# Optimization experiments

Hardware: AMD Instinct MI355X
Metric: run time of the kernel (lower is better)

The kernel has to match this reference:

```python
import jax, jax.numpy as jnp
import numpy as np


def setup_inputs() -> dict:
    key = jax.random.key(0)
    ks = jax.random.split(key, 4)
    C, Cb = 256, 32  # in_channels, bottleneck = C // 8
    B, H, W = 4, 64, 64
    x = jax.random.normal(ks[0], (B, C, H, W), dtype=jnp.float32)
    Wq = jax.random.normal(ks[1], (Cb, C), dtype=jnp.float32) * 0.05
    Wk = jax.random.normal(ks[2], (Cb, C), dtype=jnp.float32) * 0.05
    Wv = jax.random.normal(ks[3], (C, C), dtype=jnp.float32) * 0.05
    return {
        "x": x,
        "Wq": Wq, "bq": jnp.zeros((Cb,), jnp.float32),
        "Wk": Wk, "bk": jnp.zeros((Cb,), jnp.float32),
        "Wv": Wv, "bv": jnp.zeros((C,), jnp.float32),
    }


def reference(x, Wq, bq, Wk, bk, Wv, bv):
    B, C, H, W = x.shape
    N = H * W
    xf = x.reshape(B, C, N)  # [B, C, N]
    # 1x1 convs == channel matmuls
    q = jnp.einsum('oc,bcn->bon', Wq, xf) + bq[None, :, None]  # [B, Cb, N]
    k = jnp.einsum('oc,bcn->bon', Wk, xf) + bk[None, :, None]  # [B, Cb, N]
    v = jnp.einsum('oc,bcn->bon', Wv, xf) + bv[None, :, None]  # [B, C, N]
    # attention[b, n, m] = sum_d q[b, d, n] * k[b, d, m]
    attn = jnp.einsum('bdn,bdm->bnm', q, k)  # [B, N, N]
    attn = jax.nn.softmax(attn, axis=-1)
    # out[b, c, n] = sum_m v[b, c, m] * attn[b, m, n]
    out = jnp.einsum('bcm,bmn->bcn', v, attn).reshape(B, C, H, W)
    return out + x
```

## Files before the change

### kernel.cpp

```cpp
#include <hip/hip_runtime.h>
#include <hip/hip_bf16.h>

#define B_  4
#define C_  256
#define CB_ 32
#define N_  4096

typedef short bf16x8 __attribute__((ext_vector_type(8)));
typedef float f32x4  __attribute__((ext_vector_type(4)));
typedef float f32x16 __attribute__((ext_vector_type(16)));

static __device__ __forceinline__ bf16x8 ld_bf8(const __hip_bfloat16* p) {
    return *reinterpret_cast<const bf16x8*>(p);
}
static __device__ __forceinline__ unsigned pk2(float a, float b) {
    union { __hip_bfloat16 h[2]; unsigned u; } z;
    z.h[0] = __float2bfloat16(a); z.h[1] = __float2bfloat16(b);
    return z.u;
}


__global__ __launch_bounds__(256) void wconv(
    const float* __restrict__ Wq, const float* __restrict__ Wk,
    const float* __restrict__ Wv, __hip_bfloat16* __restrict__ Wc)
{
    int idx = (blockIdx.x * 256 + threadIdx.x) * 4;
    if (idx >= 320 * 256) return;
    int o = idx >> 8, c = idx & 255;
    const float* src = o < 32 ? Wq + o * 256 + c
                     : o < 64 ? Wk + (o - 32) * 256 + c
                              : Wv + (o - 64) * 256 + c;
    float4 f = *reinterpret_cast<const float4*>(src);
    union { __hip_bfloat16 h[4]; uint2 u; } pk;
    pk.h[0] = __float2bfloat16(f.x); pk.h[1] = __float2bfloat16(f.y);
    pk.h[2] = __float2bfloat16(f.z); pk.h[3] = __float2bfloat16(f.w);
    *reinterpret_cast<uint2*>(Wc + idx) = pk.u;
}

__global__ __launch_bounds__(256) void qkv_gemm(
    const float* __restrict__ x, const __hip_bfloat16* __restrict__ Wc,
    const float* __restrict__ bq, const float* __restrict__ bk,
    const float* __restrict__ bv,
    __hip_bfloat16* __restrict__ qt, __hip_bfloat16* __restrict__ kt,
    __hip_bfloat16* __restrict__ v)
{
    const int b = blockIdx.y, n0 = blockIdx.x * 32;
    const int tid = threadIdx.x, lane = tid & 63, w = tid >> 6;
    const int lg = lane >> 4, lr = lane & 15;
    __shared__ __attribute__((aligned(16))) __hip_bfloat16 T[2][32][40];
    const float* xb = x + (size_t)b * C_ * N_;

    f32x4 acc[5][2] = {};
    for (int s = 0; s < 8; ++s) {
        const int c0 = s * 32, buf = s & 1;
        {
            int cl = tid >> 3, n4 = (tid & 7) * 4;
            float4 f = *reinterpret_cast<const float4*>(
                &xb[(size_t)(c0 + cl) * N_ + n0 + n4]);
            T[buf][n4 + 0][cl] = __float2bfloat16(f.x);
            T[buf][n4 + 1][cl] = __float2bfloat16(f.y);
            T[buf][n4 + 2][cl] = __float2bfloat16(f.z);
            T[buf][n4 + 3][cl] = __float2bfloat16(f.w);
        }
        __syncthreads();
        bf16x8 bfr[2];
#pragma unroll
        for (int nf = 0; nf < 2; ++nf)
            bfr[nf] = *reinterpret_cast<const bf16x8*>(&T[buf][nf * 16 + lr][lg * 8]);
#pragma unroll
        for (int t = 0; t < 5; ++t) {
            const int of = w + 4 * t;
            bf16x8 af = ld_bf8(Wc + (size_t)(of * 16 + lr) * 256 + c0 + lg * 8);
#pragma unroll
            for (int nf = 0; nf < 2; ++nf)
                acc[t][nf] = __builtin_amdgcn_mfma_f32_16x16x32_bf16(af, bfr[nf], acc[t][nf], 0, 0, 0);
        }
        __syncthreads();
    }
#pragma unroll
    for (int t = 0; t < 5; ++t) {
        const int of = w + 4 * t, ob = of * 16 + lg * 4;
        float bias[4];
#pragma unroll
        for (int i = 0; i < 4; ++i) {
            int o = ob + i;
            bias[i] = o < 32 ? bq[o] : o < 64 ? bk[o - 32] : bv[o - 64];
        }
#pragma unroll
        for (int nf = 0; nf < 2; ++nf) {
            const int n = n0 + nf * 16 + lr;
            if (ob < 64) {
                union { __hip_bfloat16 h[4]; uint2 u; } pk;
#pragma unroll
                for (int i = 0; i < 4; ++i)
                    pk.h[i] = __float2bfloat16(acc[t][nf][i] + bias[i]);
                __hip_bfloat16* dst = ob < 32
                    ? qt + ((size_t)b * N_ + n) * CB_ + ob
                    : kt + ((size_t)b * N_ + n) * CB_ + (ob - 32);
                *reinterpret_cast<uint2*>(dst) = pk.u;
            } else {
                const size_t pbase = ((size_t)(b * (N_ / 32) + (n0 >> 5)) * C_);
#pragma unroll
                for (int i = 0; i < 4; ++i)
                    v[(pbase + (ob - 64 + i)) * 32 + nf * 16 + lr] =
                        __float2bfloat16(acc[t][nf][i] + bias[i]);
            }
        }
    }
}

__global__ __launch_bounds__(256) void row_stats_part(
    const __hip_bfloat16* __restrict__ qt, const __hip_bfloat16* __restrict__ kt,
    float* __restrict__ pM, float* __restrict__ pZ)
{
    const int m0 = blockIdx.x * 64, s = blockIdx.y, b = blockIdx.z;
    const int tid = threadIdx.x, lane = tid & 63, w = tid >> 6;
    const int lg = lane >> 4, lr = lane & 15;
    const __hip_bfloat16* qtb = qt + (size_t)b * N_ * CB_;
    const __hip_bfloat16* ktb = kt + (size_t)b * N_ * CB_;
    const int mrow = m0 + w * 16;
    bf16x8 qf = ld_bf8(qtb + (size_t)(mrow + lr) * CB_ + lg * 8);
    float rm[4] = {-1e30f, -1e30f, -1e30f, -1e30f};
    float rz[4] = {0.f, 0.f, 0.f, 0.f};
    const f32x4 zero = {0.f, 0.f, 0.f, 0.f};
    const int nbeg = s * (N_ / 4);
    for (int n = nbeg; n < nbeg + N_ / 4; n += 64) {
        f32x4 sf[4];
#pragma unroll
        for (int nf = 0; nf < 4; ++nf) {
            bf16x8 kf = ld_bf8(ktb + (size_t)(n + nf * 16 + lr) * CB_ + lg * 8);
            sf[nf] = __builtin_amdgcn_mfma_f32_16x16x32_bf16(qf, kf, zero, 0, 0, 0);
        }
#pragma unroll
        for (int i = 0; i < 4; ++i) {
            float tm = fmaxf(fmaxf(sf[0][i], sf[1][i]), fmaxf(sf[2][i], sf[3][i]));
            if (tm > rm[i]) { rz[i] *= __expf(rm[i] - tm); rm[i] = tm; }
            rz[i] += __expf(sf[0][i] - rm[i]) + __expf(sf[1][i] - rm[i]) +
                     __expf(sf[2][i] - rm[i]) + __expf(sf[3][i] - rm[i]);
        }
    }
#pragma unroll
    for (int off = 1; off < 16; off <<= 1) {
#pragma unroll
        for (int i = 0; i < 4; ++i) {
            float om = __shfl_xor(rm[i], off);
            float oz = __shfl_xor(rz[i], off);
            float nm = fmaxf(rm[i], om);
            rz[i] = rz[i] * __expf(rm[i] - nm) + oz * __expf(om - nm);
            rm[i] = nm;
        }
    }
    if (lr == 0) {
        const size_t base = ((size_t)s * B_ + b) * N_ + mrow + lg * 4;
#pragma unroll
        for (int i = 0; i < 4; ++i) { pM[base + i] = rm[i]; pZ[base + i] = rz[i]; }
    }
}

__global__ __launch_bounds__(256) void stats_combine(
    const float* __restrict__ pM, const float* __restrict__ pZ,
    float* __restrict__ rowE)
{
    const int i = blockIdx.x * 256 + threadIdx.x;
    const int BN = B_ * N_;
    float m0 = pM[i], m1 = pM[BN + i], m2 = pM[2 * BN + i], m3 = pM[3 * BN + i];
    float M = fmaxf(fmaxf(m0, m1), fmaxf(m2, m3));
    float Z = pZ[i]          * __expf(m0 - M) + pZ[BN + i]     * __expf(m1 - M)
            + pZ[2 * BN + i] * __expf(m2 - M) + pZ[3 * BN + i] * __expf(m3 - M);
    rowE[i] = M + logf(Z);
}

#define QS 4096
#define VS 32768

#define PV_BODY(qC0, qC1, vC, qN0, qN1, vN, qpN, vpN, DO_LOAD)                  \
  {                                                                             \
    f32x4 e0 = *reinterpret_cast<const f32x4*>(ep + mcur);                      \
    f32x4 e1 = *reinterpret_cast<const f32x4*>(ep + mcur + 8);                  \
    f32x4 e2 = *reinterpret_cast<const f32x4*>(ep + mcur + 16);                 \
    f32x4 e3 = *reinterpret_cast<const f32x4*>(ep + mcur + 24);                 \
    if (DO_LOAD) {                                                              \
      qN0 = ld_bf8(qpN); qN1 = ld_bf8(qpN + 16);                                \
      _Pragma("unroll")                                                         \
      for (int ct = 0; ct < 4; ++ct) {                                          \
        vN[ct][0] = ld_bf8(vpN[ct]); vN[ct][1] = ld_bf8(vpN[ct] + 16);          \
      }                                                                         \
      qpN += 2 * QS;                                                            \
      _Pragma("unroll")                                                         \
      for (int ct = 0; ct < 4; ++ct) vpN[ct] += 2 * VS;                         \
    }                                                                           \
    f32x16 sf = {};                                                             \
    sf = __builtin_amdgcn_mfma_f32_32x32x16_bf16(qC0, kB0, sf, 0, 0, 0);        \
    sf = __builtin_amdgcn_mfma_f32_32x32x16_bf16(qC1, kB1, sf, 0, 0, 0);        \
    unsigned W0 = pk2(__expf(sf[0]  - e0[0]), __expf(sf[1]  - e0[1]));          \
    unsigned W1 = pk2(__expf(sf[2]  - e0[2]), __expf(sf[3]  - e0[3]));          \
    unsigned W2 = pk2(__expf(sf[4]  - e1[0]), __expf(sf[5]  - e1[1]));          \
    unsigned W3 = pk2(__expf(sf[6]  - e1[2]), __expf(sf[7]  - e1[3]));          \
    unsigned W4 = pk2(__expf(sf[8]  - e2[0]), __expf(sf[9]  - e2[1]));          \
    unsigned W5 = pk2(__expf(sf[10] - e2[2]), __expf(sf[11] - e2[3]));          \
    unsigned W6 = pk2(__expf(sf[12] - e3[0]), __expf(sf[13] - e3[1]));          \
    unsigned W7 = pk2(__expf(sf[14] - e3[2]), __expf(sf[15] - e3[3]));          \
    asm("v_permlane32_swap_b32 %0, %1" : "+v"(W0), "+v"(W2));                   \
    asm("v_permlane32_swap_b32 %0, %1" : "+v"(W1), "+v"(W3));                   \
    asm("v_permlane32_swap_b32 %0, %1" : "+v"(W4), "+v"(W6));                   \
    asm("v_permlane32_swap_b32 %0, %1" : "+v"(W5), "+v"(W7));                   \
    union { unsigned u[4]; bf16x8 v8; } f0, f1;                                 \
    f0.u[0] = W0; f0.u[1] = W1; f0.u[2] = W2; f0.u[3] = W3;                     \
    f1.u[0] = W4; f1.u[1] = W5; f1.u[2] = W6; f1.u[3] = W7;                     \
    _Pragma("unroll")                                                           \
    for (int ct = 0; ct < 4; ++ct) {                                            \
      acc[ct] = __builtin_amdgcn_mfma_f32_32x32x16_bf16(vC[ct][0], f0.v8, acc[ct], 0, 0, 0); \
      acc[ct] = __builtin_amdgcn_mfma_f32_32x32x16_bf16(vC[ct][1], f1.v8, acc[ct], 0, 0, 0); \
    }                                                                           \
    mcur += 128;                                                                \
  }

__global__ __launch_bounds__(512) void pv_attn(
    const __hip_bfloat16* __restrict__ qt, const __hip_bfloat16* __restrict__ kt,
    const __hip_bfloat16* __restrict__ vv, const float* __restrict__ rowE,
    const float* __restrict__ x, float* __restrict__ out)
{
    const int bid = blockIdx.x;
    const int xcd = bid & 7, slot = bid >> 3;
    const int b = xcd >> 1, c0 = (xcd & 1) * 128, n0 = slot * 64;
    const int tid = threadIdx.x, lane = tid & 63, w = tid >> 6;
    const int ms = w >> 1, nf = w & 1;
    const int h = lane >> 5, l31 = lane & 31;
    const __hip_bfloat16* qtb = qt + (size_t)b * N_ * CB_;
    const __hip_bfloat16* ktb = kt + (size_t)b * N_ * CB_;
    const __hip_bfloat16* vbase = vv + (size_t)b * (N_ / 32) * C_ * 32;
    const float* ep = rowE + (size_t)b * N_ + 4 * h;

    bf16x8 kB0 = ld_bf8(ktb + (size_t)(n0 + nf * 32 + l31) * CB_ + h * 8);
    bf16x8 kB1 = ld_bf8(ktb + (size_t)(n0 + nf * 32 + l31) * CB_ + h * 8 + 16);

    const __hip_bfloat16* qpA = qtb + (size_t)(ms * 32 + l31) * CB_ + h * 8;
    const __hip_bfloat16* qpB = qpA + QS;
    const __hip_bfloat16* vpA[4];
    const __hip_bfloat16* vpB[4];
#pragma unroll
    for (int ct = 0; ct < 4; ++ct) {
        vpA[ct] = vbase + ((size_t)ms * C_ + c0 + ct * 32 + l31) * 32 + h * 8;
        vpB[ct] = vpA[ct] + VS;
    }

    f32x16 acc[4] = {};
    bf16x8 qA0, qA1, qB0, qB1;
    bf16x8 vA[4][2], vB[4][2];

    qA0 = ld_bf8(qpA); qA1 = ld_bf8(qpA + 16);
#pragma unroll
    for (int ct = 0; ct < 4; ++ct) {
        vA[ct][0] = ld_bf8(vpA[ct]); vA[ct][1] = ld_bf8(vpA[ct] + 16);
    }
    qpA += 2 * QS;
#pragma unroll
    for (int ct = 0; ct < 4; ++ct) vpA[ct] += 2 * VS;

    int mcur = ms * 32;
    for (int tt = 0; tt < 15; ++tt) {
        PV_BODY(qA0, qA1, vA, qB0, qB1, vB, qpB, vpB, true)
        PV_BODY(qB0, qB1, vB, qA0, qA1, vA, qpA, vpA, true)
    }
    PV_BODY(qA0, qA1, vA, qB0, qB1, vB, qpB, vpB, true)
    PV_BODY(qB0, qB1, vB, qA0, qA1, vA, qpA, vpA, false)

    __shared__ __attribute__((aligned(16))) float R[128][68];
#pragma unroll 1
    for (int p = 3; p >= 0; --p) {
        if (ms == p) {
#pragma unroll
            for (int i = 0; i < 16; ++i) {
                const int cl = (i & 3) + 8 * (i >> 2) + 4 * h;
                const int nn = nf * 32 + l31;
#pragma unroll
                for (int ct = 0; ct < 4; ++ct) {
                    if (p == 3) R[ct * 32 + cl][nn] = acc[ct][i];
                    else        R[ct * 32 + cl][nn] += acc[ct][i];
                }
            }
        }
        __syncthreads();
    }
    const int cr = tid >> 2, n16 = (tid & 3) * 16;
#pragma unroll
    for (int j = 0; j < 4; ++j) {
        f32x4 rv = *reinterpret_cast<const f32x4*>(&R[cr][n16 + 4 * j]);
        const size_t gi = ((size_t)b * C_ + c0 + cr) * N_ + n0 + n16 + 4 * j;
        f32x4 xv = *reinterpret_cast<const f32x4*>(x + gi);
        *reinterpret_cast<f32x4*>(out + gi) = rv + xv;
    }
}

extern "C" void kernel_launch(void* const* d_in, const int* in_sizes, int n_in,
                              void* d_out, int out_size, void* d_ws, size_t ws_size,
                              hipStream_t stream)
{
    const float* x  = (const float*)d_in[0];
    const float* Wq = (const float*)d_in[1];
    const float* bq = (const float*)d_in[2];
    const float* Wk = (const float*)d_in[3];
    const float* bk = (const float*)d_in[4];
    const float* Wv = (const float*)d_in[5];
    const float* bv = (const float*)d_in[6];
    float* out = (float*)d_out;

    char* ws = (char*)d_ws;
    __hip_bfloat16* Wc   = (__hip_bfloat16*)(ws);
    __hip_bfloat16* qt   = (__hip_bfloat16*)(ws + 0x040000);
    __hip_bfloat16* kt   = (__hip_bfloat16*)(ws + 0x140000);
    float*          rowE = (float*)(ws + 0x240000);
    float*          pM   = (float*)(ws + 0x250000);
    float*          pZ   = (float*)(ws + 0x290000);
    __hip_bfloat16* vw   = (__hip_bfloat16*)(ws + 0x400000);

    wconv<<<80, 256, 0, stream>>>(Wq, Wk, Wv, Wc);
    qkv_gemm<<<dim3(N_ / 32, B_), 256, 0, stream>>>(x, Wc, bq, bk, bv, qt, kt, vw);
    row_stats_part<<<dim3(N_ / 64, 4, B_), 256, 0, stream>>>(qt, kt, pM, pZ);
    stats_combine<<<B_ * N_ / 256, 256, 0, stream>>>(pM, pZ, rowE);
    pv_attn<<<512, 512, 0, stream>>>(qt, kt, vw, rowE, x, out);
}
```

Before: 163.4 us.

## Store Q/K/V in 8-element blocked layout and prefetch row stats in PV loop

Changes the Q, K and V workspace layouts to blocks of 8 contiguous bf16 values. The goal is that each lane's 16-byte fragment load in the MFMA loops falls in a contiguous, coalesced region across lanes instead of being strided by 64 bytes. The PV loop also double-buffers the rowE exponent offsets with the Q/V prefetch rather than loading them at the top of each step. All producers and consumers are updated together; the cost is more complex index arithmetic and extra registers for the eA/eB buffers.

```diff
diff --git a/kernel.cpp b/kernel.cpp
--- a/kernel.cpp
+++ b/kernel.cpp
@@ -41,8 +41,8 @@
     const float* __restrict__ x, const __hip_bfloat16* __restrict__ Wc,
     const float* __restrict__ bq, const float* __restrict__ bk,
     const float* __restrict__ bv,
-    __hip_bfloat16* __restrict__ qt, __hip_bfloat16* __restrict__ kt,
-    __hip_bfloat16* __restrict__ v)
+    __hip_bfloat16* __restrict__ q8, __hip_bfloat16* __restrict__ k8,
+    __hip_bfloat16* __restrict__ v8)
 {
     const int b = blockIdx.y, n0 = blockIdx.x * 32;
     const int tid = threadIdx.x, lane = tid & 63, w = tid >> 6;
@@ -94,32 +94,35 @@
 #pragma unroll
                 for (int i = 0; i < 4; ++i)
                     pk.h[i] = __float2bfloat16(acc[t][nf][i] + bias[i]);
-                __hip_bfloat16* dst = ob < 32
-                    ? qt + ((size_t)b * N_ + n) * CB_ + ob
-                    : kt + ((size_t)b * N_ + n) * CB_ + (ob - 32);
+                __hip_bfloat16* dst;
+                if (ob < 32)
+                    dst = q8 + ((size_t)(b * 4 + (ob >> 3)) * N_ + n) * 8 + (ob & 7);
+                else {
+                    const int ok = ob - 32;
+                    dst = k8 + ((size_t)(b * 4 + (ok >> 3)) * N_ + n) * 8 + (ok & 7);
+                }
                 *reinterpret_cast<uint2*>(dst) = pk.u;
             } else {
-                const size_t pbase = ((size_t)(b * (N_ / 32) + (n0 >> 5)) * C_);
 #pragma unroll
                 for (int i = 0; i < 4; ++i)
-                    v[(pbase + (ob - 64 + i)) * 32 + nf * 16 + lr] =
-                        __float2bfloat16(acc[t][nf][i] + bias[i]);
+                    v8[((size_t)(b * (N_ / 8) + (n >> 3)) * C_ + (ob - 64 + i)) * 8
+                       + (n & 7)] = __float2bfloat16(acc[t][nf][i] + bias[i]);
             }
         }
     }
 }
 
 __global__ __launch_bounds__(256) void row_stats_part(
-    const __hip_bfloat16* __restrict__ qt, const __hip_bfloat16* __restrict__ kt,
+    const __hip_bfloat16* __restrict__ q8, const __hip_bfloat16* __restrict__ k8,
     float* __restrict__ pM, float* __restrict__ pZ)
 {
     const int m0 = blockIdx.x * 64, s = blockIdx.y, b = blockIdx.z;
     const int tid = threadIdx.x, lane = tid & 63, w = tid >> 6;
     const int lg = lane >> 4, lr = lane & 15;
-    const __hip_bfloat16* qtb = qt + (size_t)b * N_ * CB_;
-    const __hip_bfloat16* ktb = kt + (size_t)b * N_ * CB_;
+    const __hip_bfloat16* q8b = q8 + (size_t)b * N_ * CB_;
+    const __hip_bfloat16* k8b = k8 + (size_t)b * N_ * CB_;
     const int mrow = m0 + w * 16;
-    bf16x8 qf = ld_bf8(qtb + (size_t)(mrow + lr) * CB_ + lg * 8);
+    bf16x8 qf = ld_bf8(q8b + ((size_t)lg * N_ + mrow + lr) * 8);
     float rm[4] = {-1e30f, -1e30f, -1e30f, -1e30f};
     float rz[4] = {0.f, 0.f, 0.f, 0.f};
     const f32x4 zero = {0.f, 0.f, 0.f, 0.f};
@@ -128,7 +131,7 @@
         f32x4 sf[4];
 #pragma unroll
         for (int nf = 0; nf < 4; ++nf) {
-            bf16x8 kf = ld_bf8(ktb + (size_t)(n + nf * 16 + lr) * CB_ + lg * 8);
+            bf16x8 kf = ld_bf8(k8b + ((size_t)lg * N_ + n + nf * 16 + lr) * 8);
             sf[nf] = __builtin_amdgcn_mfma_f32_16x16x32_bf16(qf, kf, zero, 0, 0, 0);
         }
 #pragma unroll
@@ -170,54 +173,48 @@
     rowE[i] = M + logf(Z);
 }
 
-#define QS 4096
-#define VS 32768
-
-#define PV_BODY(qC0, qC1, vC, qN0, qN1, vN, qpN, vpN, DO_LOAD)                  \
+#define PV_BODY(qC0, qC1, vC, eC, qN0, qN1, vN, eN, qpN0, qpN1, vpN0, vpN1, epN, DO_LOAD) \
   {                                                                             \
-    f32x4 e0 = *reinterpret_cast<const f32x4*>(ep + mcur);                      \
-    f32x4 e1 = *reinterpret_cast<const f32x4*>(ep + mcur + 8);                  \
-    f32x4 e2 = *reinterpret_cast<const f32x4*>(ep + mcur + 16);                 \
-    f32x4 e3 = *reinterpret_cast<const f32x4*>(ep + mcur + 24);                 \
     if (DO_LOAD) {                                                              \
-      qN0 = ld_bf8(qpN); qN1 = ld_bf8(qpN + 16);                                \
+      qN0 = ld_bf8(qpN0); qN1 = ld_bf8(qpN1);                                   \
       _Pragma("unroll")                                                         \
       for (int ct = 0; ct < 4; ++ct) {                                          \
-        vN[ct][0] = ld_bf8(vpN[ct]); vN[ct][1] = ld_bf8(vpN[ct] + 16);          \
+        vN[ct][0] = ld_bf8(vpN0 + ct * 256);                                    \
+        vN[ct][1] = ld_bf8(vpN1 + ct * 256);                                    \
       }                                                                         \
-      qpN += 2 * QS;                                                            \
       _Pragma("unroll")                                                         \
-      for (int ct = 0; ct < 4; ++ct) vpN[ct] += 2 * VS;                         \
+      for (int g = 0; g < 4; ++g)                                               \
+        eN[g] = *reinterpret_cast<const f32x4*>(epN + 8 * g);                   \
+      qpN0 += 2048; qpN1 += 2048; vpN0 += 65536; vpN1 += 65536; epN += 256;     \
     }                                                                           \
     f32x16 sf = {};                                                             \
     sf = __builtin_amdgcn_mfma_f32_32x32x16_bf16(qC0, kB0, sf, 0, 0, 0);        \
     sf = __builtin_amdgcn_mfma_f32_32x32x16_bf16(qC1, kB1, sf, 0, 0, 0);        \
-    unsigned W0 = pk2(__expf(sf[0]  - e0[0]), __expf(sf[1]  - e0[1]));          \
-    unsigned W1 = pk2(__expf(sf[2]  - e0[2]), __expf(sf[3]  - e0[3]));          \
-    unsigned W2 = pk2(__expf(sf[4]  - e1[0]), __expf(sf[5]  - e1[1]));          \
-    unsigned W3 = pk2(__expf(sf[6]  - e1[2]), __expf(sf[7]  - e1[3]));          \
-    unsigned W4 = pk2(__expf(sf[8]  - e2[0]), __expf(sf[9]  - e2[1]));          \
-    unsigned W5 = pk2(__expf(sf[10] - e2[2]), __expf(sf[11] - e2[3]));          \
-    unsigned W6 = pk2(__expf(sf[12] - e3[0]), __expf(sf[13] - e3[1]));          \
-    unsigned W7 = pk2(__expf(sf[14] - e3[2]), __expf(sf[15] - e3[3]));          \
+    unsigned W0 = pk2(__expf(sf[0]  - eC[0][0]), __expf(sf[1]  - eC[0][1]));    \
+    unsigned W1 = pk2(__expf(sf[2]  - eC[0][2]), __expf(sf[3]  - eC[0][3]));    \
+    unsigned W2 = pk2(__expf(sf[4]  - eC[1][0]), __expf(sf[5]  - eC[1][1]));    \
+    unsigned W3 = pk2(__expf(sf[6]  - eC[1][2]), __expf(sf[7]  - eC[1][3]));    \
+    unsigned W4 = pk2(__expf(sf[8]  - eC[2][0]), __expf(sf[9]  - eC[2][1]));    \
+    unsigned W5 = pk2(__expf(sf[10] - eC[2][2]), __expf(sf[11] - eC[2][3]));    \
+    unsigned W6 = pk2(__expf(sf[12] - eC[3][0]), __expf(sf[13] - eC[3][1]));    \
+    unsigned W7 = pk2(__expf(sf[14] - eC[3][2]), __expf(sf[15] - eC[3][3]));    \
     asm("v_permlane32_swap_b32 %0, %1" : "+v"(W0), "+v"(W2));                   \
     asm("v_permlane32_swap_b32 %0, %1" : "+v"(W1), "+v"(W3));                   \
     asm("v_permlane32_swap_b32 %0, %1" : "+v"(W4), "+v"(W6));                   \
     asm("v_permlane32_swap_b32 %0, %1" : "+v"(W5), "+v"(W7));                   \
-    union { unsigned u[4]; bf16x8 v8; } f0, f1;                                 \
+    union { unsigned u[4]; bf16x8 v8_; } f0, f1;                                \
     f0.u[0] = W0; f0.u[1] = W1; f0.u[2] = W2; f0.u[3] = W3;                     \
     f1.u[0] = W4; f1.u[1] = W5; f1.u[2] = W6; f1.u[3] = W7;                     \
     _Pragma("unroll")                                                           \
     for (int ct = 0; ct < 4; ++ct) {                                            \
-      acc[ct] = __builtin_amdgcn_mfma_f32_32x32x16_bf16(vC[ct][0], f0.v8, acc[ct], 0, 0, 0); \
-      acc[ct] = __builtin_amdgcn_mfma_f32_32x32x16_bf16(vC[ct][1], f1.v8, acc[ct], 0, 0, 0); \
+      acc[ct] = __builtin_amdgcn_mfma_f32_32x32x16_bf16(vC[ct][0], f0.v8_, acc[ct], 0, 0, 0); \
+      acc[ct] = __builtin_amdgcn_mfma_f32_32x32x16_bf16(vC[ct][1], f1.v8_, acc[ct], 0, 0, 0); \
     }                                                                           \
-    mcur += 128;                                                                \
   }
 
 __global__ __launch_bounds__(512) void pv_attn(
-    const __hip_bfloat16* __restrict__ qt, const __hip_bfloat16* __restrict__ kt,
-    const __hip_bfloat16* __restrict__ vv, const float* __restrict__ rowE,
+    const __hip_bfloat16* __restrict__ q8, const __hip_bfloat16* __restrict__ k8,
+    const __hip_bfloat16* __restrict__ v8, const float* __restrict__ rowE,
     const float* __restrict__ x, float* __restrict__ out)
 {
     const int bid = blockIdx.x;
@@ -226,44 +223,47 @@
     const int tid = threadIdx.x, lane = tid & 63, w = tid >> 6;
     const int ms = w >> 1, nf = w & 1;
     const int h = lane >> 5, l31 = lane & 31;
-    const __hip_bfloat16* qtb = qt + (size_t)b * N_ * CB_;
-    const __hip_bfloat16* ktb = kt + (size_t)b * N_ * CB_;
-    const __hip_bfloat16* vbase = vv + (size_t)b * (N_ / 32) * C_ * 32;
-    const float* ep = rowE + (size_t)b * N_ + 4 * h;
-
-    bf16x8 kB0 = ld_bf8(ktb + (size_t)(n0 + nf * 32 + l31) * CB_ + h * 8);
-    bf16x8 kB1 = ld_bf8(ktb + (size_t)(n0 + nf * 32 + l31) * CB_ + h * 8 + 16);
-
-    const __hip_bfloat16* qpA = qtb + (size_t)(ms * 32 + l31) * CB_ + h * 8;
-    const __hip_bfloat16* qpB = qpA + QS;
-    const __hip_bfloat16* vpA[4];
-    const __hip_bfloat16* vpB[4];
-#pragma unroll
-    for (int ct = 0; ct < 4; ++ct) {
-        vpA[ct] = vbase + ((size_t)ms * C_ + c0 + ct * 32 + l31) * 32 + h * 8;
-        vpB[ct] = vpA[ct] + VS;
-    }
+    const __hip_bfloat16* q8b = q8 + (size_t)b * N_ * CB_;
+    const __hip_bfloat16* k8b = k8 + (size_t)b * N_ * CB_;
+    const __hip_bfloat16* v8b = v8 + (size_t)b * (N_ / 8) * C_ * 8;
+
+    const int nrow = n0 + nf * 32 + l31;
+    bf16x8 kB0 = ld_bf8(k8b + ((size_t)h * N_ + nrow) * 8);
+    bf16x8 kB1 = ld_bf8(k8b + ((size_t)(2 + h) * N_ + nrow) * 8);
+
+    const __hip_bfloat16* qpA0 = q8b + ((size_t)h * N_ + ms * 32 + l31) * 8;
+    const __hip_bfloat16* qpA1 = q8b + ((size_t)(2 + h) * N_ + ms * 32 + l31) * 8;
+    const __hip_bfloat16* qpB0 = qpA0 + 128 * 8;
+    const __hip_bfloat16* qpB1 = qpA1 + 128 * 8;
+    const __hip_bfloat16* vpA0 = v8b + ((size_t)(ms * 4 + h) * C_ + c0 + l31) * 8;
+    const __hip_bfloat16* vpA1 = v8b + ((size_t)(ms * 4 + 2 + h) * C_ + c0 + l31) * 8;
+    const __hip_bfloat16* vpB0 = vpA0 + (size_t)16 * C_ * 8;
+    const __hip_bfloat16* vpB1 = vpA1 + (size_t)16 * C_ * 8;
+    const float* epA = rowE + (size_t)b * N_ + 4 * h + ms * 32;
+    const float* epB = epA + 128;
 
     f32x16 acc[4] = {};
     bf16x8 qA0, qA1, qB0, qB1;
     bf16x8 vA[4][2], vB[4][2];
-
-    qA0 = ld_bf8(qpA); qA1 = ld_bf8(qpA + 16);
+    f32x4 eA[4], eB[4];
+
+    qA0 = ld_bf8(qpA0); qA1 = ld_bf8(qpA1);
 #pragma unroll
     for (int ct = 0; ct < 4; ++ct) {
-        vA[ct][0] = ld_bf8(vpA[ct]); vA[ct][1] = ld_bf8(vpA[ct] + 16);
-    }
-    qpA += 2 * QS;
-#pragma unroll
-    for (int ct = 0; ct < 4; ++ct) vpA[ct] += 2 * VS;
-
-    int mcur = ms * 32;
+        vA[ct][0] = ld_bf8(vpA0 + ct * 256);
+        vA[ct][1] = ld_bf8(vpA1 + ct * 256);
+    }
+#pragma unroll
+    for (int g = 0; g < 4; ++g)
+        eA[g] = *reinterpret_cast<const f32x4*>(epA + 8 * g);
+    qpA0 += 2048; qpA1 += 2048; vpA0 += 65536; vpA1 += 65536; epA += 256;
+
     for (int tt = 0; tt < 15; ++tt) {
-        PV_BODY(qA0, qA1, vA, qB0, qB1, vB, qpB, vpB, true)
-        PV_BODY(qB0, qB1, vB, qA0, qA1, vA, qpA, vpA, true)
-    }
-    PV_BODY(qA0, qA1, vA, qB0, qB1, vB, qpB, vpB, true)
-    PV_BODY(qB0, qB1, vB, qA0, qA1, vA, qpA, vpA, false)
+        PV_BODY(qA0, qA1, vA, eA, qB0, qB1, vB, eB, qpB0, qpB1, vpB0, vpB1, epB, true)
+        PV_BODY(qB0, qB1, vB, eB, qA0, qA1, vA, eA, qpA0, qpA1, vpA0, vpA1, epA, true)
+    }
+    PV_BODY(qA0, qA1, vA, eA, qB0, qB1, vB, eB, qpB0, qpB1, vpB0, vpB1, epB, true)
+    PV_BODY(qB0, qB1, vB, eB, qA0, qA1, vA, eA, qpA0, qpA1, vpA0, vpA1, epA, false)
 
     __shared__ __attribute__((aligned(16))) float R[128][68];
 #pragma unroll 1
@@ -307,16 +307,16 @@
 
     char* ws = (char*)d_ws;
     __hip_bfloat16* Wc   = (__hip_bfloat16*)(ws);
-    __hip_bfloat16* qt   = (__hip_bfloat16*)(ws + 0x040000);
-    __hip_bfloat16* kt   = (__hip_bfloat16*)(ws + 0x140000);
+    __hip_bfloat16* q8   = (__hip_bfloat16*)(ws + 0x040000);
+    __hip_bfloat16* k8   = (__hip_bfloat16*)(ws + 0x140000);
     float*          rowE = (float*)(ws + 0x240000);
     float*          pM   = (float*)(ws + 0x250000);
     float*          pZ   = (float*)(ws + 0x290000);
-    __hip_bfloat16* vw   = (__hip_bfloat16*)(ws + 0x400000);
+    __hip_bfloat16* v8   = (__hip_bfloat16*)(ws + 0x400000);
 
     wconv<<<80, 256, 0, stream>>>(Wq, Wk, Wv, Wc);
-    qkv_gemm<<<dim3(N_ / 32, B_), 256, 0, stream>>>(x, Wc, bq, bk, bv, qt, kt, vw);
-    row_stats_part<<<dim3(N_ / 64, 4, B_), 256, 0, stream>>>(qt, kt, pM, pZ);
+    qkv_gemm<<<dim3(N_ / 32, B_), 256, 0, stream>>>(x, Wc, bq, bk, bv, q8, k8, v8);
+    row_stats_part<<<dim3(N_ / 64, 4, B_), 256, 0, stream>>>(q8, k8, pM, pZ);
     stats_combine<<<B_ * N_ / 256, 256, 0, stream>>>(pM, pZ, rowE);
-    pv_attn<<<512, 512, 0, stream>>>(qt, kt, vw, rowE, x, out);
-}
+    pv_attn<<<512, 512, 0, stream>>>(q8, k8, v8, rowE, x, out);
+}
```

Result: faster. 135.4 us (-17.2%).
